# Kernel tuning notes

Measured on AMD Instinct MI355X. Metric: run time of the kernel, lower is better.

## Reference

```python
import math
import jax, jax.numpy as jnp
import numpy as np

NUM_GAUSSIANS = 1024
WIDTH = 256
HEIGHT = 256
BG_COLOR = (0.0, 0.0, 0.0)
JITTER = 1e-6


def setup_inputs() -> dict:
    key = jax.random.key(0)
    k1, k2, k3 = jax.random.split(key, 3)
    means = jax.random.normal(k1, (NUM_GAUSSIANS, 2), dtype=jnp.float32)
    # init: randn - e (keeps exp(scales) small)
    scales = jax.random.normal(k2, (NUM_GAUSSIANS, 2), dtype=jnp.float32) - math.e
    thetas = jax.random.normal(k3, (NUM_GAUSSIANS, 1), dtype=jnp.float32)
    # init: inverse_sigmoid(0.1) with eps=1e-5
    eps = 1e-5
    inv_sig = math.log((0.1 + eps) / (1.0 - 0.1 + eps))
    opacities = jnp.full((NUM_GAUSSIANS, 1), inv_sig, dtype=jnp.float32)
    return {"means": means, "scales": scales, "thetas": thetas, "opacities": opacities}


def reference(means, scales, thetas, opacities):
    # activations
    m = jnp.tanh(means)                       # [N,2] in [-1,1]
    s = jnp.exp(scales)                       # [N,2]
    th = jax.nn.sigmoid(thetas[:, 0]) * 2.0 * jnp.pi  # [N]
    op = jax.nn.sigmoid(opacities[:, 0])      # [N]

    # covariance = R diag(s^2) R^T + jitter*I, 2x2, closed form
    c, si = jnp.cos(th), jnp.sin(th)
    s2 = s * s
    a = c * c * s2[:, 0] + si * si * s2[:, 1] + JITTER   # Sigma_00
    b = c * si * (s2[:, 0] - s2[:, 1])                    # Sigma_01
    d = si * si * s2[:, 0] + c * c * s2[:, 1] + JITTER   # Sigma_11
    det = a * d - b * b
    ia, ib, id_ = d / det, -b / det, a / det              # Sigma^{-1}

    # pixel grid over [-1,1]^2
    xs = jnp.linspace(-1.0, 1.0, WIDTH, dtype=jnp.float32)
    ys = jnp.linspace(-1.0, 1.0, HEIGHT, dtype=jnp.float32)
    X, Y = jnp.meshgrid(xs, ys)               # [H,W]

    dx = X[None] - m[:, 0, None, None]        # [N,H,W]
    dy = Y[None] - m[:, 1, None, None]        # [N,H,W]
    q = (ia[:, None, None] * dx * dx
         + 2.0 * ib[:, None, None] * dx * dy
         + id_[:, None, None] * dy * dy)      # Mahalanobis dist^2
    alpha = op[:, None, None] * jnp.exp(-0.5 * q)  # [N,H,W]

    # front-to-back alpha compositing in gaussian index order
    T = jnp.cumprod(1.0 - alpha, axis=0)      # transmittance after each gaussian
    T_excl = jnp.concatenate([jnp.ones((1, HEIGHT, WIDTH), jnp.float32), T[:-1]], axis=0)
    acc = jnp.sum(alpha * T_excl, axis=0)     # [H,W], white splats

    bg = jnp.asarray(BG_COLOR, dtype=jnp.float32)
    image = acc[..., None] + T[-1][..., None] * bg   # [H,W,3]
    return image
```

## Files before the change

kernel.cpp:

```cpp
#include <hip/hip_runtime.h>
#include <math.h>

#define NG 1024
#define NWAVES 8
#define IMG_W 256
#define IMG_H 256
#define TILE 16
#define JITTER 1e-6f
#define L2E 1.4426950408889634f
#define CULL_LOG2_EPS -15.0f

__device__ __forceinline__ float fexp2(float x)  { return __builtin_amdgcn_exp2f(x); }
__device__ __forceinline__ float flog2(float x)  { return __builtin_amdgcn_logf(x); }
__device__ __forceinline__ float frcp(float x)   { return __builtin_amdgcn_rcpf(x); }
__device__ __forceinline__ float fexp(float x)   { return fexp2(x * L2E); }
__device__ __forceinline__ float fsigmoid(float x) { return frcp(1.0f + fexp(-x)); }
__device__ __forceinline__ float ftanh(float x) {
    float t = fexp2(2.0f * L2E * x);
    return 1.0f - 2.0f * frcp(t + 1.0f);
}

__global__ __launch_bounds__(512, 2)
void gs_tiled(const float* __restrict__ means,
              const float* __restrict__ scales,
              const float* __restrict__ thetas,
              const float* __restrict__ opacities,
              float* __restrict__ out) {
    __shared__ float4 s_c0123[NG];
    __shared__ float2 s_c45[NG];
    __shared__ unsigned long long s_mask[2][NWAVES];
    __shared__ float2 s_seg[NWAVES][TILE * TILE];

    int tid  = threadIdx.x;
    int lane = tid & 63;
    int wave = tid >> 6;

    const float step = 2.0f / 255.0f;
    int tx = blockIdx.x & (IMG_W / TILE - 1);
    int ty = blockIdx.x >> 4;
    float rx0 = fmaf((float)(tx * TILE), step, -1.0f);
    float ry0 = fmaf((float)(ty * TILE), step, -1.0f);
    float rx1 = rx0 + (TILE - 1) * step;
    float ry1 = ry0 + (TILE - 1) * step;

    int nsurv = 0;
    #pragma unroll
    for (int k = 0; k < 2; ++k) {
        int g = k * 512 + tid;
        float mx = ftanh(means[2 * g]);
        float my = ftanh(means[2 * g + 1]);
        float s2x = fexp(2.0f * scales[2 * g]);
        float s2y = fexp(2.0f * scales[2 * g + 1]);
        float rev = fsigmoid(thetas[g]);
        float si = __builtin_amdgcn_sinf(rev);
        float c  = __builtin_amdgcn_cosf(rev);
        float a = c * c * s2x + si * si * s2y + JITTER;
        float b = c * si * (s2x - s2y);
        float d = si * si * s2x + c * c * s2y + JITTER;
        float inv_det = frcp(a * d - b * b);
        float c3 = -0.5f * L2E * d * inv_det;
        float c4 =  L2E * b * inv_det;
        float c5 = -0.5f * L2E * a * inv_det;
        float l2op = flog2(fsigmoid(opacities[g]));
        float c1 = -(2.0f * c3 * mx + c4 * my);
        float c2 = -(c4 * mx + 2.0f * c5 * my);
        float c0 = c3 * mx * mx + c4 * mx * my + c5 * my * my + l2op;

        float h3 = frcp(c3) * 0.5f;
        float h5 = frcp(c5) * 0.5f;
        float B0 = fmaf(c4, rx0, c2);
        float C0 = fmaf(rx0, fmaf(c3, rx0, c1), c0);
        float yv0 = fminf(fmaxf(-B0 * h5, ry0), ry1);
        float v0 = fmaf(yv0, fmaf(c5, yv0, B0), C0);
        float B1 = fmaf(c4, rx1, c2);
        float C1 = fmaf(rx1, fmaf(c3, rx1, c1), c0);
        float yv1 = fminf(fmaxf(-B1 * h5, ry0), ry1);
        float v1 = fmaf(yv1, fmaf(c5, yv1, B1), C1);
        float B2 = fmaf(c4, ry0, c1);
        float C2 = fmaf(ry0, fmaf(c5, ry0, c2), c0);
        float xv2 = fminf(fmaxf(-B2 * h3, rx0), rx1);
        float v2 = fmaf(xv2, fmaf(c3, xv2, B2), C2);
        float B3 = fmaf(c4, ry1, c1);
        float C3 = fmaf(ry1, fmaf(c5, ry1, c2), c0);
        float xv3 = fminf(fmaxf(-B3 * h3, rx0), rx1);
        float v3 = fmaf(xv3, fmaf(c3, xv3, B3), C3);
        float e2max = fmaxf(fmaxf(v0, v1), fmaxf(v2, v3));
        bool inside = (mx >= rx0) & (mx <= rx1) & (my >= ry0) & (my <= ry1);
        e2max = inside ? l2op : e2max;
        bool keep = e2max >= CULL_LOG2_EPS;

        unsigned long long bal = __ballot(keep);
        if (lane == 0) s_mask[k][wave] = bal;
        __syncthreads();

        int pos = nsurv;
        #pragma unroll
        for (int w = 0; w < NWAVES; ++w) {
            unsigned long long m = s_mask[k][w];
            if (w < wave) pos += __popcll(m);
            nsurv += __popcll(m);
        }
        pos += __popcll(bal & ((1ull << lane) - 1ull));

        if (keep) {
            s_c0123[pos] = make_float4(c0, c1, c2, c3);
            s_c45[pos]   = make_float2(c4, c5);
        }
    }
    __syncthreads();

    int Ns = nsurv;
    int sbeg = __builtin_amdgcn_readfirstlane((Ns * wave) >> 3);
    int send = __builtin_amdgcn_readfirstlane((Ns * (wave + 1)) >> 3);

    int col  = lane & 15;
    int rowg = lane >> 4;
    float x  = fmaf((float)col, step, rx0);
    float y0 = fmaf((float)(rowg * 4 + 0), step, ry0);
    float y1 = y0 + step;
    float y2 = y1 + step;
    float y3 = y2 + step;

    float acc0 = 0.f, T0 = 1.f, acc1 = 0.f, T1 = 1.f;
    float acc2 = 0.f, T2 = 1.f, acc3 = 0.f, T3 = 1.f;

    if (sbeg < send) {
        float4 q = s_c0123[sbeg];
        float2 r = s_c45[sbeg];
        #pragma unroll 8
        for (int i = sbeg; i < send; ++i) {
            float4 qn; float2 rn;
            if (i + 1 < send) { qn = s_c0123[i + 1]; rn = s_c45[i + 1]; }
            float t1 = fmaf(x, fmaf(q.w, x, q.y), q.x);
            float u  = fmaf(r.x, x, q.z);
            float e, al;
            e = fmaf(y0, fmaf(r.y, y0, u), t1); al = fexp2(e);
            acc0 = fmaf(al, T0, acc0); T0 = fmaf(-al, T0, T0);
            e = fmaf(y1, fmaf(r.y, y1, u), t1); al = fexp2(e);
            acc1 = fmaf(al, T1, acc1); T1 = fmaf(-al, T1, T1);
            e = fmaf(y2, fmaf(r.y, y2, u), t1); al = fexp2(e);
            acc2 = fmaf(al, T2, acc2); T2 = fmaf(-al, T2, T2);
            e = fmaf(y3, fmaf(r.y, y3, u), t1); al = fexp2(e);
            acc3 = fmaf(al, T3, acc3); T3 = fmaf(-al, T3, T3);
            q = qn; r = rn;
        }
    }

    int pxb = (rowg * 4) * TILE + col;
    s_seg[wave][pxb]            = make_float2(acc0, T0);
    s_seg[wave][pxb + TILE]     = make_float2(acc1, T1);
    s_seg[wave][pxb + 2 * TILE] = make_float2(acc2, T2);
    s_seg[wave][pxb + 3 * TILE] = make_float2(acc3, T3);
    __syncthreads();

    if (tid < TILE * TILE) {
        float A = 0.0f, Tt = 1.0f;
        #pragma unroll
        for (int s = 0; s < NWAVES; ++s) {
            float2 v = s_seg[s][tid];
            A = fmaf(Tt, v.x, A);
            Tt *= v.y;
        }
        int px = tx * TILE + (tid & 15);
        int py = ty * TILE + (tid >> 4);
        float* o = out + 3 * (py * IMG_W + px);
        o[0] = A;
        o[1] = A;
        o[2] = A;
    }
}

extern "C" void kernel_launch(void* const* d_in, const int* in_sizes, int n_in,
                              void* d_out, int out_size, void* d_ws, size_t ws_size,
                              hipStream_t stream) {
    const float* means     = (const float*)d_in[0];
    const float* scales    = (const float*)d_in[1];
    const float* thetas    = (const float*)d_in[2];
    const float* opacities = (const float*)d_in[3];
    float* out = (float*)d_out;

    gs_tiled<<<dim3((IMG_W / TILE) * (IMG_H / TILE)), dim3(512), 0, stream>>>(
        means, scales, thetas, opacities, out);
}
```

Before: 63.54 us.

## Halve tile height to 16x8, doubling block count with two pixels per lane

Shrinks each tile to 16x8 pixels so the grid has 512 blocks instead of 256. Each lane now handles two pixels instead of four, and the per-tile culling is tighter. The launch bound raises occupancy to 4 blocks per SM, and the means and scales loads are vectorised as float2. The aim is better CU utilisation and less wasted splat evaluation per tile. The cost is that every block redoes the per-gaussian preprocessing for all 1024 gaussians, which doubles total setup work, and the software prefetch in the inner loop is removed.

```diff
diff --git a/kernel.cpp b/kernel.cpp
--- a/kernel.cpp
+++ b/kernel.cpp
@@ -5,7 +5,9 @@
 #define NWAVES 8
 #define IMG_W 256
 #define IMG_H 256
-#define TILE 16
+#define TILE_W 16
+#define TILE_H 8
+#define NPX (TILE_W * TILE_H)
 #define JITTER 1e-6f
 #define L2E 1.4426950408889634f
 #define CULL_LOG2_EPS -15.0f
@@ -20,7 +22,7 @@
     return 1.0f - 2.0f * frcp(t + 1.0f);
 }
 
-__global__ __launch_bounds__(512, 2)
+__global__ __launch_bounds__(512, 4)
 void gs_tiled(const float* __restrict__ means,
               const float* __restrict__ scales,
               const float* __restrict__ thetas,
@@ -29,28 +31,30 @@
     __shared__ float4 s_c0123[NG];
     __shared__ float2 s_c45[NG];
     __shared__ unsigned long long s_mask[2][NWAVES];
-    __shared__ float2 s_seg[NWAVES][TILE * TILE];
+    __shared__ float2 s_seg[NWAVES][NPX];
 
     int tid  = threadIdx.x;
     int lane = tid & 63;
     int wave = tid >> 6;
 
     const float step = 2.0f / 255.0f;
-    int tx = blockIdx.x & (IMG_W / TILE - 1);
+    int tx = blockIdx.x & (IMG_W / TILE_W - 1);
     int ty = blockIdx.x >> 4;
-    float rx0 = fmaf((float)(tx * TILE), step, -1.0f);
-    float ry0 = fmaf((float)(ty * TILE), step, -1.0f);
-    float rx1 = rx0 + (TILE - 1) * step;
-    float ry1 = ry0 + (TILE - 1) * step;
+    float rx0 = fmaf((float)(tx * TILE_W), step, -1.0f);
+    float ry0 = fmaf((float)(ty * TILE_H), step, -1.0f);
+    float rx1 = rx0 + (TILE_W - 1) * step;
+    float ry1 = ry0 + (TILE_H - 1) * step;
 
     int nsurv = 0;
     #pragma unroll
     for (int k = 0; k < 2; ++k) {
         int g = k * 512 + tid;
-        float mx = ftanh(means[2 * g]);
-        float my = ftanh(means[2 * g + 1]);
-        float s2x = fexp(2.0f * scales[2 * g]);
-        float s2y = fexp(2.0f * scales[2 * g + 1]);
+        float2 mn = ((const float2*)means)[g];
+        float2 sc = ((const float2*)scales)[g];
+        float mx = ftanh(mn.x);
+        float my = ftanh(mn.y);
+        float s2x = fexp(2.0f * sc.x);
+        float s2y = fexp(2.0f * sc.y);
         float rev = fsigmoid(thetas[g]);
         float si = __builtin_amdgcn_sinf(rev);
         float c  = __builtin_amdgcn_cosf(rev);
@@ -116,44 +120,31 @@
     int col  = lane & 15;
     int rowg = lane >> 4;
     float x  = fmaf((float)col, step, rx0);
-    float y0 = fmaf((float)(rowg * 4 + 0), step, ry0);
+    float y0 = fmaf((float)(rowg * 2), step, ry0);
     float y1 = y0 + step;
-    float y2 = y1 + step;
-    float y3 = y2 + step;
 
     float acc0 = 0.f, T0 = 1.f, acc1 = 0.f, T1 = 1.f;
-    float acc2 = 0.f, T2 = 1.f, acc3 = 0.f, T3 = 1.f;
 
-    if (sbeg < send) {
-        float4 q = s_c0123[sbeg];
-        float2 r = s_c45[sbeg];
-        #pragma unroll 8
-        for (int i = sbeg; i < send; ++i) {
-            float4 qn; float2 rn;
-            if (i + 1 < send) { qn = s_c0123[i + 1]; rn = s_c45[i + 1]; }
-            float t1 = fmaf(x, fmaf(q.w, x, q.y), q.x);
-            float u  = fmaf(r.x, x, q.z);
-            float e, al;
-            e = fmaf(y0, fmaf(r.y, y0, u), t1); al = fexp2(e);
-            acc0 = fmaf(al, T0, acc0); T0 = fmaf(-al, T0, T0);
-            e = fmaf(y1, fmaf(r.y, y1, u), t1); al = fexp2(e);
-            acc1 = fmaf(al, T1, acc1); T1 = fmaf(-al, T1, T1);
-            e = fmaf(y2, fmaf(r.y, y2, u), t1); al = fexp2(e);
-            acc2 = fmaf(al, T2, acc2); T2 = fmaf(-al, T2, T2);
-            e = fmaf(y3, fmaf(r.y, y3, u), t1); al = fexp2(e);
-            acc3 = fmaf(al, T3, acc3); T3 = fmaf(-al, T3, T3);
-            q = qn; r = rn;
-        }
+    #pragma unroll 4
+    for (int i = sbeg; i < send; ++i) {
+        float4 q = s_c0123[i];
+        float2 r = s_c45[i];
+        float t1 = fmaf(x, fmaf(q.w, x, q.y), q.x);
+        float u  = fmaf(r.x, x, q.z);
+        float e0 = fmaf(y0, fmaf(r.y, y0, u), t1);
+        float a0 = fexp2(e0);
+        acc0 = fmaf(a0, T0, acc0); T0 = fmaf(-a0, T0, T0);
+        float e1 = fmaf(y1, fmaf(r.y, y1, u), t1);
+        float a1 = fexp2(e1);
+        acc1 = fmaf(a1, T1, acc1); T1 = fmaf(-a1, T1, T1);
     }
 
-    int pxb = (rowg * 4) * TILE + col;
-    s_seg[wave][pxb]            = make_float2(acc0, T0);
-    s_seg[wave][pxb + TILE]     = make_float2(acc1, T1);
-    s_seg[wave][pxb + 2 * TILE] = make_float2(acc2, T2);
-    s_seg[wave][pxb + 3 * TILE] = make_float2(acc3, T3);
+    int pxb = rowg * 2 * TILE_W + col;
+    s_seg[wave][pxb]          = make_float2(acc0, T0);
+    s_seg[wave][pxb + TILE_W] = make_float2(acc1, T1);
     __syncthreads();
 
-    if (tid < TILE * TILE) {
+    if (tid < NPX) {
         float A = 0.0f, Tt = 1.0f;
         #pragma unroll
         for (int s = 0; s < NWAVES; ++s) {
@@ -161,8 +152,8 @@
             A = fmaf(Tt, v.x, A);
             Tt *= v.y;
         }
-        int px = tx * TILE + (tid & 15);
-        int py = ty * TILE + (tid >> 4);
+        int px = tx * TILE_W + (tid & 15);
+        int py = ty * TILE_H + (tid >> 4);
         float* o = out + 3 * (py * IMG_W + px);
         o[0] = A;
         o[1] = A;
@@ -179,6 +170,6 @@
     const float* opacities = (const float*)d_in[3];
     float* out = (float*)d_out;
 
-    gs_tiled<<<dim3((IMG_W / TILE) * (IMG_H / TILE)), dim3(512), 0, stream>>>(
+    gs_tiled<<<dim3((IMG_W / TILE_W) * (IMG_H / TILE_H)), dim3(512), 0, stream>>>(
         means, scales, thetas, opacities, out);
 }
```

After: 63.35 us. About the same (-0.3%).
